# Optimization experiments

Hardware: AMD Instinct MI355X
Metric: run time of the kernel (lower is better)

Reference implementation:

```python
import jax, jax.numpy as jnp
import numpy as np

N_SAMPLES = 4096
BACKBONE_OUT = 512
EXPANSION = 8192
NUM_CLASSES = 1000
C_COEF = 1.0


def setup_inputs() -> dict:
    key = jax.random.key(0)
    k1, k2, k3, k4 = jax.random.split(key, 4)
    X = jax.random.normal(k1, (N_SAMPLES, BACKBONE_OUT), dtype=jnp.float32)
    W_buffer = jax.random.normal(k2, (BACKBONE_OUT, EXPANSION), dtype=jnp.float32) / np.sqrt(BACKBONE_OUT)
    W_main = jax.random.normal(k3, (EXPANSION, NUM_CLASSES), dtype=jnp.float32) / np.sqrt(EXPANSION)
    W_comp = jax.random.normal(k4, (EXPANSION, NUM_CLASSES), dtype=jnp.float32) / np.sqrt(EXPANSION)
    return {"X": X, "W_buffer": W_buffer, "W_main": W_main, "W_comp": W_comp, "k": 500}


def _knn_mean_cosine(Xe, k):
    # Xe: [N, D]. Cosine kNN (excluding self), then mean of neighbor features.
    N = Xe.shape[0]
    Xn = Xe / jnp.linalg.norm(Xe, axis=1, keepdims=True)
    sim = Xn @ Xn.T                                      # [N, N]
    diag = jnp.arange(N)
    sim = sim.at[diag, diag].set(-jnp.inf)               # exclude self (== indices[:,1:])
    _, idx = jax.lax.top_k(sim, k)                       # [N, k] nearest by cosine
    # Gather-mean via binary adjacency matmul (avoids [N,k,D] intermediate).
    rows = jnp.repeat(diag, k)
    A = jnp.zeros((N, N), Xe.dtype).at[rows, idx.reshape(-1)].set(1.0)
    return (A @ Xe) / jnp.asarray(k, Xe.dtype)           # [N, D]


def reference(X, W_buffer, W_main, W_comp, k):
    Xe = X @ W_buffer                                    # random buffer expansion [N, D]
    X_main = jnp.maximum(Xe, 0.0) @ W_main               # relu -> main analytic linear
    X_knn = _knn_mean_cosine(Xe, k)
    X_comp = jnp.tanh(X_knn) @ W_comp                    # tanh -> compensation linear
    return X_main + C_COEF * X_comp
```

## Files before the change

### kernel.cpp

```cpp
#include <hip/hip_runtime.h>
#include <hip/hip_bf16.h>

#define MSAMP 4096
#define D0    512
#define EXPN  8192
#define NCLS  1000
#define NPAD  1024
#define QSCALE     (6.0f / 127.0f)
#define QSCALE_INV (127.0f / 6.0f)

typedef __attribute__((ext_vector_type(8))) _Float16       half8;
typedef __attribute__((ext_vector_type(8))) unsigned short ushort8v;
typedef __attribute__((ext_vector_type(4))) float          f32x4;
typedef __attribute__((ext_vector_type(4))) int            i32x4v;

__device__ __forceinline__ unsigned short f2h(float f) {
    union { _Float16 h; unsigned short u; } c; c.h = (_Float16)f; return c.u;
}
__device__ __forceinline__ float h2f(unsigned short u) {
    union { unsigned short u; _Float16 h; } c; c.u = u; return (float)c.h;
}
__device__ __forceinline__ ushort8v relu8h(ushort8v v) {
#pragma unroll
    for (int j = 0; j < 8; ++j) v[j] = (v[j] & 0x8000u) ? (unsigned short)0 : v[j];
    return v;
}
__device__ __forceinline__ half8 as_half8(const unsigned short* p) {
    return *(const half8*)p;
}
__device__ __forceinline__ float tanh_fast(float x) {
    float e = __expf(2.0f * x);
    return 1.0f - 2.0f * __builtin_amdgcn_rcpf(e + 1.0f);
}

__global__ __launch_bounds__(256) void cvt_x(const float* __restrict__ src,
                                             unsigned short* __restrict__ dst)
{
    const size_t i = ((size_t)blockIdx.x * 256 + threadIdx.x) * 8;
    float4 v0 = *(const float4*)(src + i), v1 = *(const float4*)(src + i + 4);
    union { unsigned short u[8]; ushort8v v; } H;
    H.u[0] = f2h(v0.x); H.u[1] = f2h(v0.y); H.u[2] = f2h(v0.z); H.u[3] = f2h(v0.w);
    H.u[4] = f2h(v1.x); H.u[5] = f2h(v1.y); H.u[6] = f2h(v1.z); H.u[7] = f2h(v1.w);
    *(ushort8v*)(dst + i) = H.v;
}

__global__ void transpose_wb(const float* __restrict__ src,
                             unsigned short* __restrict__ dst)
{
    __shared__ float t[32][33];
    const int n0 = blockIdx.x * 32, k0 = blockIdx.y * 32;
    const int tx = threadIdx.x, ty = threadIdx.y;
#pragma unroll
    for (int i = 0; i < 4; ++i)
        t[ty + 8 * i][tx] = src[(size_t)(k0 + ty + 8 * i) * EXPN + n0 + tx];
    __syncthreads();
#pragma unroll
    for (int i = 0; i < 4; ++i)
        dst[(size_t)(n0 + ty + 8 * i) * D0 + k0 + tx] = f2h(t[tx][ty + 8 * i]);
}

__global__ __launch_bounds__(256) void gemm_xe_mfma(
    const unsigned short* __restrict__ Xh, const unsigned short* __restrict__ WbT,
    unsigned short* __restrict__ Xe)
{
    __shared__ __align__(16) char smem[34816];
    unsigned short (*AsF)[2][64][8] = (unsigned short (*)[2][64][8])(smem);
    unsigned short (*BsF)[2][64][8] = (unsigned short (*)[2][64][8])(smem + 16384);

    const int tid = threadIdx.x;
    const int wid = tid >> 6, lane = tid & 63;
    const int l15 = lane & 15, q = lane >> 4;
    const int wm = (wid >> 1) * 64, wn = (wid & 1) * 64;
    const int row0 = blockIdx.y * 128, col0 = blockIdx.x * 128;

    const int sr = tid >> 1;
    const int scp = (tid & 1) * 2;
    const int mi_w = sr >> 4;
    const int l_ws = (sr & 15) ^ ((tid & 1) << 2);
    const int lane_s = lane ^ ((lane >> 3) & 4);

    f32x4 acc[4][4];
#pragma unroll
    for (int m = 0; m < 4; ++m)
#pragma unroll
        for (int n = 0; n < 4; ++n) acc[m][n] = (f32x4){0.f, 0.f, 0.f, 0.f};

    for (int k0 = 0; k0 < D0; k0 += 64) {
        const unsigned short* pa = Xh  + (size_t)(row0 + sr) * D0 + k0 + scp * 8;
        const unsigned short* pb = WbT + (size_t)(col0 + sr) * D0 + k0 + scp * 8;
        ushort8v a0 = *(const ushort8v*)pa,        a1 = *(const ushort8v*)(pa + 8);
        ushort8v a2 = *(const ushort8v*)(pa + 32), a3 = *(const ushort8v*)(pa + 40);
        ushort8v b0 = *(const ushort8v*)pb,        b1 = *(const ushort8v*)(pb + 8);
        ushort8v b2 = *(const ushort8v*)(pb + 32), b3 = *(const ushort8v*)(pb + 40);

        __syncthreads();
        *(ushort8v*)&AsF[mi_w][0][scp * 16 + l_ws][0]       = a0;
        *(ushort8v*)&AsF[mi_w][0][(scp + 1) * 16 + l_ws][0] = a1;
        *(ushort8v*)&AsF[mi_w][1][scp * 16 + l_ws][0]       = a2;
        *(ushort8v*)&AsF[mi_w][1][(scp + 1) * 16 + l_ws][0] = a3;
        *(ushort8v*)&BsF[mi_w][0][scp * 16 + l_ws][0]       = b0;
        *(ushort8v*)&BsF[mi_w][0][(scp + 1) * 16 + l_ws][0] = b1;
        *(ushort8v*)&BsF[mi_w][1][scp * 16 + l_ws][0]       = b2;
        *(ushort8v*)&BsF[mi_w][1][(scp + 1) * 16 + l_ws][0] = b3;
        __syncthreads();

        half8 fa[4][2], fb[4][2];
#pragma unroll
        for (int m = 0; m < 4; ++m) {
            fa[m][0] = as_half8(&AsF[(wm >> 4) + m][0][lane_s][0]);
            fa[m][1] = as_half8(&AsF[(wm >> 4) + m][1][lane_s][0]);
            fb[m][0] = as_half8(&BsF[(wn >> 4) + m][0][lane_s][0]);
            fb[m][1] = as_half8(&BsF[(wn >> 4) + m][1][lane_s][0]);
        }
#pragma unroll
        for (int m = 0; m < 4; ++m)
#pragma unroll
            for (int n = 0; n < 4; ++n) {
                acc[m][n] = __builtin_amdgcn_mfma_f32_16x16x32_f16(fa[m][0], fb[n][0], acc[m][n], 0, 0, 0);
                acc[m][n] = __builtin_amdgcn_mfma_f32_16x16x32_f16(fa[m][1], fb[n][1], acc[m][n], 0, 0, 0);
            }
    }

    unsigned short (*Cb)[136] = (unsigned short (*)[136])smem;
    const int rr = tid >> 1, hh = (tid & 1) * 64;
    __syncthreads();
#pragma unroll
    for (int m = 0; m < 4; ++m)
#pragma unroll
        for (int n = 0; n < 4; ++n)
#pragma unroll
            for (int r = 0; r < 4; ++r)
                Cb[wm + m * 16 + q * 4 + r][wn + n * 16 + l15] = f2h(acc[m][n][r]);
    __syncthreads();
#pragma unroll
    for (int c = 0; c < 8; ++c)
        *(ushort8v*)&Xe[(size_t)(row0 + rr) * EXPN + col0 + hh + c * 8] =
            *(const ushort8v*)&Cb[rr][hh + c * 8];
}

__global__ __launch_bounds__(256) void gemm_sim(
    const unsigned short* __restrict__ Xe,
    const float* __restrict__ invn, float* __restrict__ Sm)
{
    __shared__ unsigned short AsF[8][2][64][8], BsF[8][2][64][8];

    const int t = blockIdx.x;
    int bj = (int)((sqrtf(8.0f * t + 1.0f) - 1.0f) * 0.5f);
    while ((bj + 1) * (bj + 2) / 2 <= t) ++bj;
    while (bj * (bj + 1) / 2 > t) --bj;
    const int bi = t - bj * (bj + 1) / 2;
    const int row0 = bi * 128, col0 = bj * 128;

    const int tid = threadIdx.x;
    const int wid = tid >> 6, lane = tid & 63;
    const int l15 = lane & 15, q = lane >> 4;
    const int wm = (wid >> 1) * 64, wn = (wid & 1) * 64;

    const int sr = tid >> 1;
    const int scp = (tid & 1) * 2;
    const int mi_w = sr >> 4;
    const int l_ws = (sr & 15) ^ ((tid & 1) << 2);
    const int lane_s = lane ^ ((lane >> 3) & 4);

    f32x4 acc[4][4];
#pragma unroll
    for (int m = 0; m < 4; ++m)
#pragma unroll
        for (int n = 0; n < 4; ++n) acc[m][n] = (f32x4){0.f, 0.f, 0.f, 0.f};

    for (int k0 = 0; k0 < EXPN; k0 += 64) {
        const unsigned short* pa = Xe + (size_t)(row0 + sr) * EXPN + k0 + scp * 8;
        const unsigned short* pb = Xe + (size_t)(col0 + sr) * EXPN + k0 + scp * 8;
        ushort8v a0 = *(const ushort8v*)pa,        a1 = *(const ushort8v*)(pa + 8);
        ushort8v a2 = *(const ushort8v*)(pa + 32), a3 = *(const ushort8v*)(pa + 40);
        ushort8v b0 = *(const ushort8v*)pb,        b1 = *(const ushort8v*)(pb + 8);
        ushort8v b2 = *(const ushort8v*)(pb + 32), b3 = *(const ushort8v*)(pb + 40);

        __syncthreads();
        *(ushort8v*)&AsF[mi_w][0][scp * 16 + l_ws][0]       = a0;
        *(ushort8v*)&AsF[mi_w][0][(scp + 1) * 16 + l_ws][0] = a1;
        *(ushort8v*)&AsF[mi_w][1][scp * 16 + l_ws][0]       = a2;
        *(ushort8v*)&AsF[mi_w][1][(scp + 1) * 16 + l_ws][0] = a3;
        *(ushort8v*)&BsF[mi_w][0][scp * 16 + l_ws][0]       = b0;
        *(ushort8v*)&BsF[mi_w][0][(scp + 1) * 16 + l_ws][0] = b1;
        *(ushort8v*)&BsF[mi_w][1][scp * 16 + l_ws][0]       = b2;
        *(ushort8v*)&BsF[mi_w][1][(scp + 1) * 16 + l_ws][0] = b3;
        __syncthreads();

        half8 fa[4][2], fb[4][2];
#pragma unroll
        for (int m = 0; m < 4; ++m) {
            fa[m][0] = as_half8(&AsF[(wm >> 4) + m][0][lane_s][0]);
            fa[m][1] = as_half8(&AsF[(wm >> 4) + m][1][lane_s][0]);
            fb[m][0] = as_half8(&BsF[(wn >> 4) + m][0][lane_s][0]);
            fb[m][1] = as_half8(&BsF[(wn >> 4) + m][1][lane_s][0]);
        }
#pragma unroll
        for (int m = 0; m < 4; ++m)
#pragma unroll
            for (int n = 0; n < 4; ++n) {
                acc[m][n] = __builtin_amdgcn_mfma_f32_16x16x32_f16(fa[m][0], fb[n][0], acc[m][n], 0, 0, 0);
                acc[m][n] = __builtin_amdgcn_mfma_f32_16x16x32_f16(fa[m][1], fb[n][1], acc[m][n], 0, 0, 0);
            }
    }

    const bool mirror = (bi != bj);
#pragma unroll
    for (int m = 0; m < 4; ++m)
#pragma unroll
        for (int n = 0; n < 4; ++n) {
            const int gj = col0 + wn + n * 16 + l15;
            const float invj = invn[gj];
#pragma unroll
            for (int r = 0; r < 4; ++r) {
                const int gi = row0 + wm + m * 16 + q * 4 + r;
                float v = acc[m][n][r] * invn[gi] * invj;
                if (gi == gj) v = -3.0e38f;
                Sm[(size_t)gi * MSAMP + gj] = v;
                if (mirror) Sm[(size_t)gj * MSAMP + gi] = v;
            }
        }
}

__global__ __launch_bounds__(256) void gemm_adj_i8(
    const unsigned* __restrict__ Abits, const signed char* __restrict__ XeT,
    unsigned short* __restrict__ Tk, const int* __restrict__ kp)
{
    __shared__ signed char BsF[8][2][64][16];
    __shared__ uint4 aw4[128];

    const int tid = threadIdx.x;
    const int wid = tid >> 6, lane = tid & 63;
    const int l15 = lane & 15, q = lane >> 4;
    const int wm = (wid >> 1) * 64, wn = (wid & 1) * 64;

    const int orig = blockIdx.x + blockIdx.y * 32;
    const int s = (orig & 7) * 256 + (orig >> 3);
    const int row0 = (s & 31) * 128;
    const int col0 = (s >> 5) * 128;

    const int sr = tid >> 1;
    const int half = tid & 1;
    const int l_ws = (sr & 15) ^ (half << 2);
    const int lane_s = lane ^ ((lane >> 3) & 4);

    i32x4v acc[4][4];
#pragma unroll
    for (int m = 0; m < 4; ++m)
#pragma unroll
        for (int n = 0; n < 4; ++n) acc[m][n] = (i32x4v){0, 0, 0, 0};

    for (int k0 = 0; k0 < MSAMP; k0 += 128) {
        const signed char* pb = XeT + (size_t)(col0 + sr) * MSAMP + k0 + half * 32;
        i32x4v b0 = *(const i32x4v*)pb;
        i32x4v b1 = *(const i32x4v*)(pb + 16);
        i32x4v b2 = *(const i32x4v*)(pb + 64);
        i32x4v b3 = *(const i32x4v*)(pb + 80);
        uint4 wv = make_uint4(0u, 0u, 0u, 0u);
        if (tid < 128)
            wv = *(const uint4*)(Abits + (size_t)(row0 + tid) * (MSAMP / 32) + (k0 >> 5));

        __syncthreads();
        *(i32x4v*)&BsF[sr >> 4][0][(half * 2 + 0) * 16 + l_ws][0] = b0;
        *(i32x4v*)&BsF[sr >> 4][0][(half * 2 + 1) * 16 + l_ws][0] = b1;
        *(i32x4v*)&BsF[sr >> 4][1][(half * 2 + 0) * 16 + l_ws][0] = b2;
        *(i32x4v*)&BsF[sr >> 4][1][(half * 2 + 1) * 16 + l_ws][0] = b3;
        if (tid < 128) aw4[tid] = wv;
        __syncthreads();

        i32x4v fb[4][2];
#pragma unroll
        for (int n = 0; n < 4; ++n) {
            fb[n][0] = *(const i32x4v*)&BsF[(wn >> 4) + n][0][lane_s][0];
            fb[n][1] = *(const i32x4v*)&BsF[(wn >> 4) + n][1][lane_s][0];
        }

#pragma unroll
        for (int m = 0; m < 4; ++m) {
            const uint4 ww = aw4[wm + m * 16 + l15];
#pragma unroll
            for (int kh = 0; kh < 2; ++kh) {
                const unsigned w = (kh == 0) ? ((q >= 2) ? ww.y : ww.x)
                                             : ((q >= 2) ? ww.w : ww.z);
                const unsigned hw = (q & 1) ? (w >> 16) : w;
                i32x4v fa;
#pragma unroll
                for (int p = 0; p < 4; ++p)
                    fa[p] = (int)((((hw >> (4 * p)) & 0xFu) * 0x00204081u) & 0x01010101u);
#pragma unroll
                for (int n = 0; n < 4; ++n)
                    acc[m][n] = __builtin_amdgcn_mfma_i32_16x16x64_i8(fa, fb[n][kh], acc[m][n], 0, 0, 0);
            }
        }
    }

    const float kv = QSCALE / (float)(*kp);
#pragma unroll
    for (int m = 0; m < 4; ++m)
#pragma unroll
        for (int n = 0; n < 4; ++n) {
            const int gj = col0 + wn + n * 16 + l15;
#pragma unroll
            for (int r = 0; r < 4; ++r) {
                const int gi = row0 + wm + m * 16 + q * 4 + r;
                Tk[(size_t)gi * EXPN + gj] = f2h(tanh_fast((float)acc[m][n][r] * kv));
            }
        }
}

__global__ void transpose_w(const float* __restrict__ src,
                            unsigned short* __restrict__ dst)
{
    __shared__ float t[32][33];
    const int k0 = blockIdx.x * 32, n0 = blockIdx.y * 32;
    const int tx = threadIdx.x, ty = threadIdx.y;
#pragma unroll
    for (int i = 0; i < 4; ++i) {
        const int n = n0 + tx;
        t[ty + 8 * i][tx] = (n < NCLS) ? src[(size_t)(k0 + ty + 8 * i) * NCLS + n] : 0.f;
    }
    __syncthreads();
#pragma unroll
    for (int i = 0; i < 4; ++i)
        dst[(size_t)(n0 + ty + 8 * i) * EXPN + k0 + tx] = f2h(t[tx][ty + 8 * i]);
}

__global__ __launch_bounds__(256) void gemm_out_split(
    const unsigned short* __restrict__ Xe, const unsigned short* __restrict__ Tk,
    const unsigned short* __restrict__ WmT, const unsigned short* __restrict__ WcT,
    float* __restrict__ Cout, unsigned short* __restrict__ Pf)
{
    __shared__ unsigned short AsF[8][2][64][8], BsF[8][2][64][8];

    const int tid = threadIdx.x;
    const int wid = tid >> 6, lane = tid & 63;
    const int l15 = lane & 15, q = lane >> 4;
    const int wm = (wid >> 1) * 64, wn = (wid & 1) * 64;

    const int orig = blockIdx.x + blockIdx.y * 8;
    const int s = (orig & 7) * 32 + (orig >> 3);
    const int col0 = (s & 7) * 128;
    const int row0 = (s >> 3) * 128;
    const int zz = blockIdx.z;
    const bool xe_side = (zz < 2);
    const int kbase = (zz & 1) * (EXPN / 2);

    const unsigned short* Abase = xe_side ? Xe : Tk;
    const unsigned short* Bbase = xe_side ? WmT : WcT;

    const int sr = tid >> 1;
    const int scp = (tid & 1) * 2;
    const int mi_w = sr >> 4;
    const int l_ws = (sr & 15) ^ ((tid & 1) << 2);
    const int lane_s = lane ^ ((lane >> 3) & 4);

    f32x4 acc[4][4];
#pragma unroll
    for (int m = 0; m < 4; ++m)
#pragma unroll
        for (int n = 0; n < 4; ++n) acc[m][n] = (f32x4){0.f, 0.f, 0.f, 0.f};

    for (int kk = 0; kk < EXPN / 2; kk += 64) {
        const int k0 = kbase + kk;
        const unsigned short* pa = Abase + (size_t)(row0 + sr) * EXPN + k0 + scp * 8;
        const unsigned short* pb = Bbase + (size_t)(col0 + sr) * EXPN + k0 + scp * 8;
        ushort8v a0 = *(const ushort8v*)pa,        a1 = *(const ushort8v*)(pa + 8);
        ushort8v a2 = *(const ushort8v*)(pa + 32), a3 = *(const ushort8v*)(pa + 40);
        ushort8v b0 = *(const ushort8v*)pb,        b1 = *(const ushort8v*)(pb + 8);
        ushort8v b2 = *(const ushort8v*)(pb + 32), b3 = *(const ushort8v*)(pb + 40);
        if (xe_side) { a0 = relu8h(a0); a1 = relu8h(a1); a2 = relu8h(a2); a3 = relu8h(a3); }

        __syncthreads();
        *(ushort8v*)&AsF[mi_w][0][scp * 16 + l_ws][0]       = a0;
        *(ushort8v*)&AsF[mi_w][0][(scp + 1) * 16 + l_ws][0] = a1;
        *(ushort8v*)&AsF[mi_w][1][scp * 16 + l_ws][0]       = a2;
        *(ushort8v*)&AsF[mi_w][1][(scp + 1) * 16 + l_ws][0] = a3;
        *(ushort8v*)&BsF[mi_w][0][scp * 16 + l_ws][0]       = b0;
        *(ushort8v*)&BsF[mi_w][0][(scp + 1) * 16 + l_ws][0] = b1;
        *(ushort8v*)&BsF[mi_w][1][scp * 16 + l_ws][0]       = b2;
        *(ushort8v*)&BsF[mi_w][1][(scp + 1) * 16 + l_ws][0] = b3;
        __syncthreads();

        half8 fa[4][2], fb[4][2];
#pragma unroll
        for (int m = 0; m < 4; ++m) {
            fa[m][0] = as_half8(&AsF[(wm >> 4) + m][0][lane_s][0]);
            fa[m][1] = as_half8(&AsF[(wm >> 4) + m][1][lane_s][0]);
            fb[m][0] = as_half8(&BsF[(wn >> 4) + m][0][lane_s][0]);
            fb[m][1] = as_half8(&BsF[(wn >> 4) + m][1][lane_s][0]);
        }
#pragma unroll
        for (int m = 0; m < 4; ++m)
#pragma unroll
            for (int n = 0; n < 4; ++n) {
                acc[m][n] = __builtin_amdgcn_mfma_f32_16x16x32_f16(fa[m][0], fb[n][0], acc[m][n], 0, 0, 0);
                acc[m][n] = __builtin_amdgcn_mfma_f32_16x16x32_f16(fa[m][1], fb[n][1], acc[m][n], 0, 0, 0);
            }
    }

    if (zz == 0) {
#pragma unroll
        for (int m = 0; m < 4; ++m)
#pragma unroll
            for (int n = 0; n < 4; ++n) {
                const int gj = col0 + wn + n * 16 + l15;
                if (gj < NCLS) {
#pragma unroll
                    for (int r = 0; r < 4; ++r) {
                        const int gi = row0 + wm + m * 16 + q * 4 + r;
                        Cout[(size_t)gi * NCLS + gj] = acc[m][n][r];
                    }
                }
            }
    } else {
        unsigned short* dp = Pf + (size_t)(zz - 1) * MSAMP * NCLS;
#pragma unroll
        for (int m = 0; m < 4; ++m)
#pragma unroll
            for (int n = 0; n < 4; ++n) {
                const int gj = col0 + wn + n * 16 + l15;
                if (gj < NCLS) {
#pragma unroll
                    for (int r = 0; r < 4; ++r) {
                        const int gi = row0 + wm + m * 16 + q * 4 + r;
                        dp[(size_t)gi * NCLS + gj] = f2h(acc[m][n][r]);
                    }
                }
            }
    }
}

__global__ __launch_bounds__(256) void add_partials(float* __restrict__ out,
                                                    const unsigned short* __restrict__ P,
                                                    int n4)
{
    const int i = blockIdx.x * 256 + threadIdx.x;
    if (i < n4) {
        float4 a = ((const float4*)out)[i];
        const ushort4 p0 = *(const ushort4*)(P + (size_t)i * 4);
        const ushort4 p1 = *(const ushort4*)(P + (size_t)MSAMP * NCLS + (size_t)i * 4);
        const ushort4 p2 = *(const ushort4*)(P + (size_t)2 * MSAMP * NCLS + (size_t)i * 4);
        a.x += h2f(p0.x) + h2f(p1.x) + h2f(p2.x);
        a.y += h2f(p0.y) + h2f(p1.y) + h2f(p2.y);
        a.z += h2f(p0.z) + h2f(p1.z) + h2f(p2.z);
        a.w += h2f(p0.w) + h2f(p1.w) + h2f(p2.w);
        ((float4*)out)[i] = a;
    }
}

__global__ __launch_bounds__(256) void row_invnorm(
    const unsigned short* __restrict__ Xe, float* __restrict__ invn)
{
    const int row = blockIdx.x;
    float s = 0.f;
    for (int j = threadIdx.x * 8; j < EXPN; j += 2048) {
        ushort8v h = *(const ushort8v*)(Xe + (size_t)row * EXPN + j);
#pragma unroll
        for (int c = 0; c < 8; ++c) { float x = h2f(h[c]); s += x * x; }
    }
#pragma unroll
    for (int off = 32; off > 0; off >>= 1) s += __shfl_down(s, off);
    __shared__ float wsum[4];
    if ((threadIdx.x & 63) == 0) wsum[threadIdx.x >> 6] = s;
    __syncthreads();
    if (threadIdx.x == 0)
        invn[row] = rsqrtf(wsum[0] + wsum[1] + wsum[2] + wsum[3]);
}

__global__ __launch_bounds__(256) void topk_thresh(const float* __restrict__ sim,
                                                   float* __restrict__ thr,
                                                   int N, const int* __restrict__ kp)
{
    const int row = blockIdx.x;
    const float* srow = sim + (size_t)row * N;
    __shared__ int hist[256];
    __shared__ unsigned s_prefix;
    __shared__ int s_rem;
    if (threadIdx.x == 0) { s_prefix = 0u; s_rem = *kp; }
    __syncthreads();

    for (int pass = 0; pass < 4; ++pass) {
        const int shift = 24 - 8 * pass;
        hist[threadIdx.x] = 0;
        __syncthreads();
        const unsigned prefix = s_prefix;
        const unsigned pmask = (pass == 0) ? 0u : (0xFFFFFFFFu << (shift + 8));
        for (int j = threadIdx.x; j < N; j += 256) {
            unsigned u = __float_as_uint(srow[j]);
            u = ((int)u < 0) ? ~u : (u | 0x80000000u);
            if ((u & pmask) == (prefix & pmask))
                atomicAdd(&hist[(u >> shift) & 255], 1);
        }
        __syncthreads();
        if (threadIdx.x == 0) {
            int rem = s_rem, accum = 0, b;
            for (b = 255; b > 0; --b) {
                if (accum + hist[b] >= rem) break;
                accum += hist[b];
            }
            s_rem = rem - accum;
            s_prefix = prefix | ((unsigned)b << shift);
        }
        __syncthreads();
    }

    if (threadIdx.x == 0) {
        const unsigned u = s_prefix;
        const unsigned orig = (u & 0x80000000u) ? (u & 0x7FFFFFFFu) : ~u;
        thr[row] = __uint_as_float(orig);
    }
}

__global__ __launch_bounds__(128) void bitpack(const float* __restrict__ Sm,
                                               const float* __restrict__ thr,
                                               unsigned* __restrict__ Abits)
{
    const int row = blockIdx.x;
    const int w = threadIdx.x;
    const float t = thr[row];
    const float* p = Sm + (size_t)row * MSAMP + w * 32;
    unsigned m = 0;
#pragma unroll
    for (int b = 0; b < 32; b += 4) {
        float4 v = *(const float4*)(p + b);
        m |= (v.x >= t ? 1u : 0u) << (b + 0);
        m |= (v.y >= t ? 1u : 0u) << (b + 1);
        m |= (v.z >= t ? 1u : 0u) << (b + 2);
        m |= (v.w >= t ? 1u : 0u) << (b + 3);
    }
    Abits[(size_t)row * (MSAMP / 32) + w] = m;
}

__global__ void transpose_xe_q(const unsigned short* __restrict__ src,
                               signed char* __restrict__ dst)
{
    __shared__ signed char t[32][36];
    const int bx = blockIdx.x;
    const int by = blockIdx.y;
    const int tx = threadIdx.x, ty = threadIdx.y;
#pragma unroll
    for (int i = 0; i < 4; ++i) {
        float v = h2f(src[(size_t)(by * 32 + ty + 8 * i) * EXPN + bx * 32 + tx]);
        int qv = (int)rintf(v * QSCALE_INV);
        qv = max(-127, min(127, qv));
        t[tx][ty + 8 * i] = (signed char)qv;
    }
    __syncthreads();
    const int tid = ty * 32 + tx;
    const int nl = tid >> 3, mg = (tid & 7) * 4;
    char4 o;
    o.x = t[nl][mg + 0]; o.y = t[nl][mg + 1];
    o.z = t[nl][mg + 2]; o.w = t[nl][mg + 3];
    *(char4*)&dst[(size_t)(bx * 32 + nl) * MSAMP + by * 32 + mg] = o;
}

extern "C" void kernel_launch(void* const* d_in, const int* in_sizes, int n_in,
                              void* d_out, int out_size, void* d_ws, size_t ws_size,
                              hipStream_t stream)
{
    const float* X  = (const float*)d_in[0];
    const float* Wb = (const float*)d_in[1];
    const float* Wm = (const float*)d_in[2];
    const float* Wc = (const float*)d_in[3];
    const int*   kp = (const int*)d_in[4];
    float* out = (float*)d_out;

    char* base = (char*)d_ws;
    const size_t SEG = (size_t)64 << 20;
    const size_t need = 3 * SEG + ((size_t)2 << 20) + 65536;
    if (ws_size < need) return;

    unsigned short* Xe   = (unsigned short*)base;
    signed char*    XeTq = (signed char*)(base + SEG);
    unsigned short* WmT  = (unsigned short*)(base + SEG);
    unsigned short* WcT  = WmT + (size_t)NPAD * EXPN;
    unsigned short* Pf   = (unsigned short*)(base + SEG + ((size_t)32 << 20));
    unsigned short* Xh   = (unsigned short*)(base + 2 * SEG);
    unsigned short* WbT  = Xh + (size_t)MSAMP * D0;
    float*          Sm   = (float*)(base + 2 * SEG);
    unsigned short* Tk   = (unsigned short*)(base + 2 * SEG);
    unsigned*       Abits= (unsigned*)(base + 3 * SEG);
    float*          invn = (float*)(base + 3 * SEG + ((size_t)2 << 20));
    float*          thr  = invn + MSAMP;

    const dim3 blk(256);

    cvt_x<<<dim3((MSAMP * D0) / (256 * 8)), blk, 0, stream>>>(X, Xh);
    transpose_wb<<<dim3(EXPN / 32, D0 / 32), dim3(32, 8), 0, stream>>>(Wb, WbT);

    gemm_xe_mfma<<<dim3(EXPN / 128, MSAMP / 128), blk, 0, stream>>>(Xh, WbT, Xe);

    row_invnorm<<<dim3(MSAMP), blk, 0, stream>>>(Xe, invn);

    gemm_sim<<<dim3(528), blk, 0, stream>>>(Xe, invn, Sm);

    topk_thresh<<<dim3(MSAMP), blk, 0, stream>>>(Sm, thr, MSAMP, kp);

    bitpack<<<dim3(MSAMP), dim3(128), 0, stream>>>(Sm, thr, Abits);

    transpose_xe_q<<<dim3(EXPN / 32, MSAMP / 32), dim3(32, 8), 0, stream>>>(Xe, XeTq);

    gemm_adj_i8<<<dim3(MSAMP / 128, EXPN / 128), blk, 0, stream>>>(Abits, XeTq, Tk, kp);

    transpose_w<<<dim3(EXPN / 32, NPAD / 32), dim3(32, 8), 0, stream>>>(Wm, WmT);
    transpose_w<<<dim3(EXPN / 32, NPAD / 32), dim3(32, 8), 0, stream>>>(Wc, WcT);

    gemm_out_split<<<dim3(NPAD / 128, MSAMP / 128, 4), blk, 0, stream>>>(
        Xe, Tk, WmT, WcT, out, Pf);

    add_partials<<<dim3((MSAMP * NCLS / 4 + 255) / 256), blk, 0, stream>>>(
        out, Pf, MSAMP * NCLS / 4);
}
```

Baseline: 894.2 us.

## Split similarity GEMM along K into two halves with a combine kernel

The symmetric similarity GEMM now launches two K-halves per triangular tile, which doubles the grid from 528 blocks so more compute units stay busy. The first half writes raw partial sums into the similarity matrix and the second writes them into a scratch buffer. A new combine kernel adds the halves, applies the inverse norms, masks the diagonal and writes the mirrored transpose. The cost is extra global traffic for the partials, one more launch, and scattered strided mirror stores in the combine.

```diff
diff --git a/kernel.cpp b/kernel.cpp
--- a/kernel.cpp
+++ b/kernel.cpp
@@ -139,17 +139,19 @@
 }
 
 __global__ __launch_bounds__(256) void gemm_sim(
-    const unsigned short* __restrict__ Xe,
-    const float* __restrict__ invn, float* __restrict__ Sm)
+    const unsigned short* __restrict__ Xe, float* __restrict__ Sm,
+    float* __restrict__ P1)
 {
     __shared__ unsigned short AsF[8][2][64][8], BsF[8][2][64][8];
 
     const int t = blockIdx.x;
+    const int kh = blockIdx.y;
     int bj = (int)((sqrtf(8.0f * t + 1.0f) - 1.0f) * 0.5f);
     while ((bj + 1) * (bj + 2) / 2 <= t) ++bj;
     while (bj * (bj + 1) / 2 > t) --bj;
     const int bi = t - bj * (bj + 1) / 2;
     const int row0 = bi * 128, col0 = bj * 128;
+    const int kbase = kh * (EXPN / 2);
 
     const int tid = threadIdx.x;
     const int wid = tid >> 6, lane = tid & 63;
@@ -168,7 +170,8 @@
 #pragma unroll
         for (int n = 0; n < 4; ++n) acc[m][n] = (f32x4){0.f, 0.f, 0.f, 0.f};
 
-    for (int k0 = 0; k0 < EXPN; k0 += 64) {
+    for (int kk = 0; kk < EXPN / 2; kk += 64) {
+        const int k0 = kbase + kk;
         const unsigned short* pa = Xe + (size_t)(row0 + sr) * EXPN + k0 + scp * 8;
         const unsigned short* pb = Xe + (size_t)(col0 + sr) * EXPN + k0 + scp * 8;
         ushort8v a0 = *(const ushort8v*)pa,        a1 = *(const ushort8v*)(pa + 8);
@@ -204,22 +207,76 @@
             }
     }
 
+    if (kh == 0) {
+#pragma unroll
+        for (int m = 0; m < 4; ++m)
+#pragma unroll
+            for (int n = 0; n < 4; ++n) {
+                const int gj = col0 + wn + n * 16 + l15;
+#pragma unroll
+                for (int r = 0; r < 4; ++r) {
+                    const int gi = row0 + wm + m * 16 + q * 4 + r;
+                    Sm[(size_t)gi * MSAMP + gj] = acc[m][n][r];
+                }
+            }
+    } else {
+        float* dp = P1 + (size_t)t * 16384;
+#pragma unroll
+        for (int m = 0; m < 4; ++m)
+#pragma unroll
+            for (int n = 0; n < 4; ++n) {
+                const int lj = wn + n * 16 + l15;
+#pragma unroll
+                for (int r = 0; r < 4; ++r) {
+                    const int li = wm + m * 16 + q * 4 + r;
+                    dp[li * 128 + lj] = acc[m][n][r];
+                }
+            }
+    }
+}
+
+__global__ __launch_bounds__(256) void sim_combine(
+    float* __restrict__ Sm, const float* __restrict__ P1,
+    const float* __restrict__ invn)
+{
+    const int t = blockIdx.x;
+    int bj = (int)((sqrtf(8.0f * t + 1.0f) - 1.0f) * 0.5f);
+    while ((bj + 1) * (bj + 2) / 2 <= t) ++bj;
+    while (bj * (bj + 1) / 2 > t) --bj;
+    const int bi = t - bj * (bj + 1) / 2;
+    const int row0 = bi * 128, col0 = bj * 128;
+
+    const int r  = threadIdx.x >> 1;
+    const int c0 = (threadIdx.x & 1) * 64;
+    const int gi = row0 + r;
+    const float invi = invn[gi];
     const bool mirror = (bi != bj);
-#pragma unroll
-    for (int m = 0; m < 4; ++m)
-#pragma unroll
-        for (int n = 0; n < 4; ++n) {
-            const int gj = col0 + wn + n * 16 + l15;
-            const float invj = invn[gj];
-#pragma unroll
-            for (int r = 0; r < 4; ++r) {
-                const int gi = row0 + wm + m * 16 + q * 4 + r;
-                float v = acc[m][n][r] * invn[gi] * invj;
-                if (gi == gj) v = -3.0e38f;
-                Sm[(size_t)gi * MSAMP + gj] = v;
-                if (mirror) Sm[(size_t)gj * MSAMP + gi] = v;
-            }
-        }
+
+    float* srow = Sm + (size_t)gi * MSAMP + col0 + c0;
+    const float* prow = P1 + (size_t)t * 16384 + r * 128 + c0;
+
+#pragma unroll
+    for (int i = 0; i < 16; ++i) {
+        float4 a  = *(const float4*)(srow + i * 4);
+        float4 b  = *(const float4*)(prow + i * 4);
+        float4 nj = *(const float4*)(invn + col0 + c0 + i * 4);
+        float v0 = (a.x + b.x) * invi * nj.x;
+        float v1 = (a.y + b.y) * invi * nj.y;
+        float v2 = (a.z + b.z) * invi * nj.z;
+        float v3 = (a.w + b.w) * invi * nj.w;
+        const int gj0 = col0 + c0 + i * 4;
+        if (gi == gj0 + 0) v0 = -3.0e38f;
+        if (gi == gj0 + 1) v1 = -3.0e38f;
+        if (gi == gj0 + 2) v2 = -3.0e38f;
+        if (gi == gj0 + 3) v3 = -3.0e38f;
+        *(float4*)(srow + i * 4) = make_float4(v0, v1, v2, v3);
+        if (mirror) {
+            Sm[(size_t)(gj0 + 0) * MSAMP + gi] = v0;
+            Sm[(size_t)(gj0 + 1) * MSAMP + gi] = v1;
+            Sm[(size_t)(gj0 + 2) * MSAMP + gi] = v2;
+            Sm[(size_t)(gj0 + 3) * MSAMP + gi] = v3;
+        }
+    }
 }
 
 __global__ __launch_bounds__(256) void gemm_adj_i8(
@@ -571,6 +628,7 @@
     if (ws_size < need) return;
 
     unsigned short* Xe   = (unsigned short*)base;
+    float*          SimP1= (float*)(base + SEG);
     signed char*    XeTq = (signed char*)(base + SEG);
     unsigned short* WmT  = (unsigned short*)(base + SEG);
     unsigned short* WcT  = WmT + (size_t)NPAD * EXPN;
@@ -592,7 +650,8 @@
 
     row_invnorm<<<dim3(MSAMP), blk, 0, stream>>>(Xe, invn);
 
-    gemm_sim<<<dim3(528), blk, 0, stream>>>(Xe, invn, Sm);
+    gemm_sim<<<dim3(528, 2), blk, 0, stream>>>(Xe, Sm, SimP1);
+    sim_combine<<<dim3(528), blk, 0, stream>>>(Sm, SimP1, invn);
 
     topk_thresh<<<dim3(MSAMP), blk, 0, stream>>>(Sm, thr, MSAMP, kp);
 
```

New measurement: 1.042 ms. 16.6% more time.

## Double-buffer LDS tiles and prefetch next K-slice in similarity GEMM

Applied to the files above, without the earlier changes.

The similarity GEMM now keeps two LDS buffers and issues the next K-step's global loads into registers right after the barrier, before the MFMA work on the current tile. Global load latency can then overlap with compute, and one of the two barriers per iteration is removed. The cost is double the LDS footprint and more live registers, which may lower occupancy.

```diff
diff --git a/kernel.cpp b/kernel.cpp
--- a/kernel.cpp
+++ b/kernel.cpp
@@ -142,7 +142,7 @@
     const unsigned short* __restrict__ Xe,
     const float* __restrict__ invn, float* __restrict__ Sm)
 {
-    __shared__ unsigned short AsF[8][2][64][8], BsF[8][2][64][8];
+    __shared__ unsigned short AsF[2][8][2][64][8], BsF[2][8][2][64][8];
 
     const int t = blockIdx.x;
     int bj = (int)((sqrtf(8.0f * t + 1.0f) - 1.0f) * 0.5f);
@@ -162,38 +162,47 @@
     const int l_ws = (sr & 15) ^ ((tid & 1) << 2);
     const int lane_s = lane ^ ((lane >> 3) & 4);
 
+    const unsigned short* pa0 = Xe + (size_t)(row0 + sr) * EXPN + scp * 8;
+    const unsigned short* pb0 = Xe + (size_t)(col0 + sr) * EXPN + scp * 8;
+
     f32x4 acc[4][4];
 #pragma unroll
     for (int m = 0; m < 4; ++m)
 #pragma unroll
         for (int n = 0; n < 4; ++n) acc[m][n] = (f32x4){0.f, 0.f, 0.f, 0.f};
 
+    ushort8v a0 = *(const ushort8v*)pa0,        a1 = *(const ushort8v*)(pa0 + 8);
+    ushort8v a2 = *(const ushort8v*)(pa0 + 32), a3 = *(const ushort8v*)(pa0 + 40);
+    ushort8v b0 = *(const ushort8v*)pb0,        b1 = *(const ushort8v*)(pb0 + 8);
+    ushort8v b2 = *(const ushort8v*)(pb0 + 32), b3 = *(const ushort8v*)(pb0 + 40);
+
+    int p = 0;
     for (int k0 = 0; k0 < EXPN; k0 += 64) {
-        const unsigned short* pa = Xe + (size_t)(row0 + sr) * EXPN + k0 + scp * 8;
-        const unsigned short* pb = Xe + (size_t)(col0 + sr) * EXPN + k0 + scp * 8;
-        ushort8v a0 = *(const ushort8v*)pa,        a1 = *(const ushort8v*)(pa + 8);
-        ushort8v a2 = *(const ushort8v*)(pa + 32), a3 = *(const ushort8v*)(pa + 40);
-        ushort8v b0 = *(const ushort8v*)pb,        b1 = *(const ushort8v*)(pb + 8);
-        ushort8v b2 = *(const ushort8v*)(pb + 32), b3 = *(const ushort8v*)(pb + 40);
-
-        __syncthreads();
-        *(ushort8v*)&AsF[mi_w][0][scp * 16 + l_ws][0]       = a0;
-        *(ushort8v*)&AsF[mi_w][0][(scp + 1) * 16 + l_ws][0] = a1;
-        *(ushort8v*)&AsF[mi_w][1][scp * 16 + l_ws][0]       = a2;
-        *(ushort8v*)&AsF[mi_w][1][(scp + 1) * 16 + l_ws][0] = a3;
-        *(ushort8v*)&BsF[mi_w][0][scp * 16 + l_ws][0]       = b0;
-        *(ushort8v*)&BsF[mi_w][0][(scp + 1) * 16 + l_ws][0] = b1;
-        *(ushort8v*)&BsF[mi_w][1][scp * 16 + l_ws][0]       = b2;
-        *(ushort8v*)&BsF[mi_w][1][(scp + 1) * 16 + l_ws][0] = b3;
-        __syncthreads();
+        *(ushort8v*)&AsF[p][mi_w][0][scp * 16 + l_ws][0]       = a0;
+        *(ushort8v*)&AsF[p][mi_w][0][(scp + 1) * 16 + l_ws][0] = a1;
+        *(ushort8v*)&AsF[p][mi_w][1][scp * 16 + l_ws][0]       = a2;
+        *(ushort8v*)&AsF[p][mi_w][1][(scp + 1) * 16 + l_ws][0] = a3;
+        *(ushort8v*)&BsF[p][mi_w][0][scp * 16 + l_ws][0]       = b0;
+        *(ushort8v*)&BsF[p][mi_w][0][(scp + 1) * 16 + l_ws][0] = b1;
+        *(ushort8v*)&BsF[p][mi_w][1][scp * 16 + l_ws][0]       = b2;
+        *(ushort8v*)&BsF[p][mi_w][1][(scp + 1) * 16 + l_ws][0] = b3;
+        __syncthreads();
+
+        if (k0 + 64 < EXPN) {
+            const int kn = k0 + 64;
+            a0 = *(const ushort8v*)(pa0 + kn);        a1 = *(const ushort8v*)(pa0 + kn + 8);
+            a2 = *(const ushort8v*)(pa0 + kn + 32);   a3 = *(const ushort8v*)(pa0 + kn + 40);
+            b0 = *(const ushort8v*)(pb0 + kn);        b1 = *(const ushort8v*)(pb0 + kn + 8);
+            b2 = *(const ushort8v*)(pb0 + kn + 32);   b3 = *(const ushort8v*)(pb0 + kn + 40);
+        }
 
         half8 fa[4][2], fb[4][2];
 #pragma unroll
         for (int m = 0; m < 4; ++m) {
-            fa[m][0] = as_half8(&AsF[(wm >> 4) + m][0][lane_s][0]);
-            fa[m][1] = as_half8(&AsF[(wm >> 4) + m][1][lane_s][0]);
-            fb[m][0] = as_half8(&BsF[(wn >> 4) + m][0][lane_s][0]);
-            fb[m][1] = as_half8(&BsF[(wn >> 4) + m][1][lane_s][0]);
+            fa[m][0] = as_half8(&AsF[p][(wm >> 4) + m][0][lane_s][0]);
+            fa[m][1] = as_half8(&AsF[p][(wm >> 4) + m][1][lane_s][0]);
+            fb[m][0] = as_half8(&BsF[p][(wn >> 4) + m][0][lane_s][0]);
+            fb[m][1] = as_half8(&BsF[p][(wn >> 4) + m][1][lane_s][0]);
         }
 #pragma unroll
         for (int m = 0; m < 4; ++m)
@@ -202,6 +211,7 @@
                 acc[m][n] = __builtin_amdgcn_mfma_f32_16x16x32_f16(fa[m][0], fb[n][0], acc[m][n], 0, 0, 0);
                 acc[m][n] = __builtin_amdgcn_mfma_f32_16x16x32_f16(fa[m][1], fb[n][1], acc[m][n], 0, 0, 0);
             }
+        p ^= 1;
     }
 
     const bool mirror = (bi != bj);
```

Result: slower. 923.6 us (+3.3%).
